# Kernel tuning notes

Hardware: AMD Instinct MI355X
Metric: run time of the kernel (lower is better)

Reference implementation:

```python
import jax, jax.numpy as jnp
import numpy as np

NSTEPS = 8  # scaling-and-squaring steps
SHAPE = (2, 3, 160, 192, 160)  # (batch, ndim, D, H, W)


def _pull3d_wrap(img, coords):
    """Trilinear grid_pull with 'dft' (circular) bound, extrapolate=False.

    img:    (B, D, H, W, C) values
    coords: (B, D, H, W, 3) sampling coordinates in voxels (z, y, x order)
    """
    B, D, H, W, C = img.shape
    c0 = jnp.floor(coords)
    f = coords - c0                       # fractional part, differentiable
    c0 = c0.astype(jnp.int32)
    img_flat = img.reshape(B, D * H * W, C)
    out = jnp.zeros_like(img)
    for dz in (0, 1):
        wz = f[..., 0] if dz else (1.0 - f[..., 0])
        z = jnp.mod(c0[..., 0] + dz, D)
        for dy in (0, 1):
            wy = f[..., 1] if dy else (1.0 - f[..., 1])
            y = jnp.mod(c0[..., 1] + dy, H)
            for dx in (0, 1):
                wx = f[..., 2] if dx else (1.0 - f[..., 2])
                x = jnp.mod(c0[..., 2] + dx, W)
                idx = (z * H + y) * W + x          # (B, D, H, W)
                vals = jnp.take_along_axis(img_flat, idx.reshape(B, -1, 1), axis=1)
                vals = vals.reshape(B, D, H, W, C)
                out = out + vals * (wz * wy * wx)[..., None]
    # extrapolate=False: zero where sample lies outside voxel centers [0, n-1]
    nmax = jnp.asarray([D - 1, H - 1, W - 1], dtype=coords.dtype)
    inb = jnp.all((coords >= 0.0) & (coords <= nmax), axis=-1)
    return jnp.where(inb[..., None], out, 0.0)


def setup_inputs() -> dict:
    key = jax.random.key(0)
    flow = jax.random.normal(key, SHAPE, dtype=jnp.float32)
    return {"flow": flow}


def reference(flow) -> jnp.ndarray:
    """FlowExp forward (interpolation='linear', bound='dft', extrapolate=False,
    coeff=False). Linear spline coefficients == values, so ValueToCoeff /
    CoeffToValue are identities and the loop is pure composition:
        v <- grid_pull(v, identity_grid + v)
    """
    v = jnp.moveaxis(flow, 1, -1) / (2 ** NSTEPS)   # (B, D, H, W, 3)
    B, D, H, W, _ = v.shape
    gz, gy, gx = jnp.meshgrid(
        jnp.arange(D, dtype=v.dtype),
        jnp.arange(H, dtype=v.dtype),
        jnp.arange(W, dtype=v.dtype),
        indexing="ij",
    )
    grid = jnp.stack([gz, gy, gx], axis=-1)          # identity grid (D,H,W,3)
    for _ in range(NSTEPS):
        v = _pull3d_wrap(v, grid[None] + v)
    return jnp.moveaxis(v, -1, 1)                    # (B, 3, D, H, W)
```

## Files before the change

### kernel.cpp

```cpp
#include <hip/hip_runtime.h>


#define BB 2
#define DD 160
#define HH 192
#define WW 160

constexpr int HW    = HH * WW;
constexpr int PLANE = DD * HW;
constexpr int TX = 32, TY = 8, TZ = 8;
constexpr int SX = TX + 2, SY = TY + 2, SZ = TZ + 2;
constexpr int SYX  = SY * SX;
constexpr int SLICE   = 3 * SYX;
constexpr int SLICE_P = 1024;
constexpr int LDSF = SZ * SLICE_P;

constexpr int GX = WW / TX;
constexpr int GY = HH / TY;
constexpr int GZ = (DD / TZ) * BB;
constexpr int NBLK  = GX * GY * GZ;
constexpr int CHUNK = NBLK / 8;

__device__ __forceinline__ void gld_lds4(const float* g, float* l) {
    __builtin_amdgcn_global_load_lds(
        (const __attribute__((address_space(1))) void*)g,
        (__attribute__((address_space(3))) void*)l, 4, 0, 0);
}

__device__ __forceinline__ void tile_coords(int& x0, int& y0, int& z0, int& b) {
    const int lid = blockIdx.x + GX * (blockIdx.y + GY * blockIdx.z);
    const int nl  = (lid & 7) * CHUNK + (lid >> 3);
    const int bx  = nl % GX;
    int r = nl / GX;
    const int by  = r % GY;
    r /= GY;
    b  = r / (DD / TZ);
    x0 = bx * TX;
    y0 = by * TY;
    z0 = (r % (DD / TZ)) * TZ;
}

__device__ __forceinline__ int row_term(int syi, int sxi, int x0, int y0,
                                        bool border) {
    if (!border) return (y0 - 1 + syi) * WW + (x0 - 1 + sxi);
    const int gy = min(max(y0 - 1 + syi, 0), HH - 1);
    const int gx = min(max(x0 - 1 + sxi, 0), WW - 1);
    return gy * WW + gx;
}

__global__ __launch_bounds__(256, 4) void flow_first(const float* __restrict__ vin,
                                                     float* __restrict__ vout,
                                                     float scale) {
    __shared__ float lds[LDSF];
    const int tid = threadIdx.x;
    int x0, y0, z0, b;
    tile_coords(x0, y0, z0, b);
    const bool border = (x0 == 0) | (x0 + TX >= WW) |
                        (y0 == 0) | (y0 + TY >= HH) |
                        (z0 == 0) | (z0 + TZ >= DD);
    const float* vb = vin + b * 3 * PLANE;

    int g0, g1, g2, g3;
    {
        const int l0 = tid;
        int v = l0 / 3, c = l0 - v * 3, a = v / SX;
        g0 = c * PLANE + row_term(a, v - a * SX, x0, y0, border);
        const int l1 = tid + 256;
        v = l1 / 3; c = l1 - v * 3; a = v / SX;
        g1 = c * PLANE + row_term(a, v - a * SX, x0, y0, border);
        const int l2 = tid + 512;
        v = l2 / 3; c = l2 - v * 3; a = v / SX;
        g2 = c * PLANE + row_term(a, v - a * SX, x0, y0, border);
        const int l3 = min(tid + 768, SLICE - 1);
        v = l3 / 3; c = l3 - v * 3; a = v / SX;
        g3 = c * PLANE + row_term(a, v - a * SX, x0, y0, border);
    }

    #pragma unroll
    for (int szi = 0; szi < SZ; ++szi) {
        int zb = z0 - 1 + szi;
        if (border) zb = min(max(zb, 0), DD - 1);
        const float* sp = vb + zb * HW;
        float* lb = lds + szi * SLICE_P;
        gld_lds4(sp + g0, lb + tid);
        gld_lds4(sp + g1, lb + tid + 256);
        gld_lds4(sp + g2, lb + tid + 512);
        gld_lds4(sp + g3, lb + tid + 768);
    }
    __syncthreads();

    const int tx = tid & (TX - 1), ty = tid >> 5;
    const int x = x0 + tx, y = y0 + ty;
    #pragma unroll 2
    for (int zz = 0; zz < TZ; ++zz) {
        const int z = z0 + zz;
        const int so = (zz + 1) * SLICE_P + 3 * ((ty + 1) * SX + (tx + 1));
        const float vz = lds[so] * scale;
        const float vy = lds[so + 1] * scale;
        const float vx = lds[so + 2] * scale;
        const float cz = (float)z + vz, cy = (float)y + vy, cx = (float)x + vx;
        const bool jz = vz < 0.f, jy = vy < 0.f, jx = vx < 0.f;
        const float gzf = jz ? vz + 1.f : vz;
        const float gyf = jy ? vy + 1.f : vy;
        const float gxf = jx ? vx + 1.f : vx;
        const bool inb = (cz >= 0.f) & (cz <= (float)(DD - 1)) &
                         (cy >= 0.f) & (cy <= (float)(HH - 1)) &
                         (cx >= 0.f) & (cx <= (float)(WW - 1));
        const float m = inb ? 1.f : 0.f;
        const float wz1 = gzf * m, wz0 = m - wz1;
        const float wy1 = gyf, wy0 = 1.f - gyf;
        const float wx1 = gxf, wx0 = 1.f - gxf;
        const int sb = ((so - (jx ? 3 : 0)) - (jy ? 3 * SX : 0))
                       - (jz ? SLICE_P : 0);
        float oz = 0.f, oy = 0.f, ox = 0.f;
        #pragma unroll
        for (int dz = 0; dz < 2; ++dz) {
            const float wzv = dz ? wz1 : wz0;
            #pragma unroll
            for (int dy = 0; dy < 2; ++dy) {
                const float wzy = wzv * (dy ? wy1 : wy0);
                const float w0 = wzy * wx0, w1 = wzy * wx1;
                const int o = sb + dz * SLICE_P + dy * (3 * SX);
                oz += lds[o]     * w0; oy += lds[o + 1] * w0; ox += lds[o + 2] * w0;
                oz += lds[o + 3] * w1; oy += lds[o + 4] * w1; ox += lds[o + 5] * w1;
            }
        }
        float t[3] = { oz * scale, oy * scale, ox * scale };
        __builtin_memcpy(vout + (((b * DD + z) * HH + y) * WW + x) * 3, t, 12);
    }
}

template<int OUT_PLANAR>
__global__ __launch_bounds__(256, 4) void flow_mid(const float* __restrict__ vin,
                                                   float* __restrict__ vout) {
    __shared__ float lds[LDSF];
    const int tid = threadIdx.x;
    int x0, y0, z0, b;
    tile_coords(x0, y0, z0, b);
    const bool border = (x0 == 0) | (x0 + TX >= WW) |
                        (y0 == 0) | (y0 + TY >= HH) |
                        (z0 == 0) | (z0 + TZ >= DD);
    const float* vb = vin + b * PLANE * 3;

    int g0, g1, g2, g3;
    {
        const int l0 = tid;
        int v = l0 / 3, c = l0 - v * 3, a = v / SX;
        g0 = row_term(a, v - a * SX, x0, y0, border) * 3 + c;
        const int l1 = tid + 256;
        v = l1 / 3; c = l1 - v * 3; a = v / SX;
        g1 = row_term(a, v - a * SX, x0, y0, border) * 3 + c;
        const int l2 = tid + 512;
        v = l2 / 3; c = l2 - v * 3; a = v / SX;
        g2 = row_term(a, v - a * SX, x0, y0, border) * 3 + c;
        const int l3 = min(tid + 768, SLICE - 1);
        v = l3 / 3; c = l3 - v * 3; a = v / SX;
        g3 = row_term(a, v - a * SX, x0, y0, border) * 3 + c;
    }

    #pragma unroll
    for (int szi = 0; szi < SZ; ++szi) {
        int zb = z0 - 1 + szi;
        if (border) zb = min(max(zb, 0), DD - 1);
        const float* sp = vb + zb * (HW * 3);
        float* lb = lds + szi * SLICE_P;
        gld_lds4(sp + g0, lb + tid);
        gld_lds4(sp + g1, lb + tid + 256);
        gld_lds4(sp + g2, lb + tid + 512);
        gld_lds4(sp + g3, lb + tid + 768);
    }
    __syncthreads();

    const int tx = tid & (TX - 1), ty = tid >> 5;
    const int x = x0 + tx, y = y0 + ty;
    #pragma unroll 2
    for (int zz = 0; zz < TZ; ++zz) {
        const int z = z0 + zz;
        const int so = (zz + 1) * SLICE_P + 3 * ((ty + 1) * SX + (tx + 1));
        const float vz = lds[so], vy = lds[so + 1], vx = lds[so + 2];
        const float cz = (float)z + vz, cy = (float)y + vy, cx = (float)x + vx;
        const bool jz = vz < 0.f, jy = vy < 0.f, jx = vx < 0.f;
        const float gzf = jz ? vz + 1.f : vz;
        const float gyf = jy ? vy + 1.f : vy;
        const float gxf = jx ? vx + 1.f : vx;
        const bool inb = (cz >= 0.f) & (cz <= (float)(DD - 1)) &
                         (cy >= 0.f) & (cy <= (float)(HH - 1)) &
                         (cx >= 0.f) & (cx <= (float)(WW - 1));
        const float m = inb ? 1.f : 0.f;
        const float wz1 = gzf * m, wz0 = m - wz1;
        const float wy1 = gyf, wy0 = 1.f - gyf;
        const float wx1 = gxf, wx0 = 1.f - gxf;
        const int sb = ((so - (jx ? 3 : 0)) - (jy ? 3 * SX : 0))
                       - (jz ? SLICE_P : 0);
        float oz = 0.f, oy = 0.f, ox = 0.f;
        #pragma unroll
        for (int dz = 0; dz < 2; ++dz) {
            const float wzv = dz ? wz1 : wz0;
            #pragma unroll
            for (int dy = 0; dy < 2; ++dy) {
                const float wzy = wzv * (dy ? wy1 : wy0);
                const float w0 = wzy * wx0, w1 = wzy * wx1;
                const int o = sb + dz * SLICE_P + dy * (3 * SX);
                oz += lds[o]     * w0; oy += lds[o + 1] * w0; ox += lds[o + 2] * w0;
                oz += lds[o + 3] * w1; oy += lds[o + 4] * w1; ox += lds[o + 5] * w1;
            }
        }
        if (OUT_PLANAR) {
            float* op = vout + b * 3 * PLANE + (z * HH + y) * WW + x;
            op[0] = oz; op[PLANE] = oy; op[2 * PLANE] = ox;
        } else {
            float t[3] = { oz, oy, ox };
            __builtin_memcpy(vout + (((b * DD + z) * HH + y) * WW + x) * 3, t, 12);
        }
    }
}

extern "C" void kernel_launch(void* const* d_in, const int* in_sizes, int n_in,
                              void* d_out, int out_size, void* d_ws, size_t ws_size,
                              hipStream_t stream) {
    const float* flow = (const float*)d_in[0];
    float* out = (float*)d_out;
    float* wsA = (float*)d_ws;

    dim3 blk(256);
    dim3 grd(GX, GY, GZ);
    const float s = 1.f / 256.f;

    flow_first<<<grd, blk, 0, stream>>>(flow, wsA, s);
    flow_mid<0><<<grd, blk, 0, stream>>>(wsA, out);
    flow_mid<0><<<grd, blk, 0, stream>>>(out, wsA);
    flow_mid<0><<<grd, blk, 0, stream>>>(wsA, out);
    flow_mid<0><<<grd, blk, 0, stream>>>(out, wsA);
    flow_mid<0><<<grd, blk, 0, stream>>>(wsA, out);
    flow_mid<0><<<grd, blk, 0, stream>>>(out, wsA);
    flow_mid<1><<<grd, blk, 0, stream>>>(wsA, out);
}
```

Measured before the change: 397.6 us.

## Pad LDS halo to float4 per voxel and halve z-tile depth

Changes the shared-memory halo layout from 3 floats per voxel to 4, so each corner fetch in the trilinear gather becomes one 16-byte LDS read instead of three scalar reads. To stay within the LDS budget, the z tile depth drops from 8 to 4, which doubles the block count and raises the halo overhead ratio (6 loaded slices per 4 output slices). The gather and store code is factored into a shared template, and the z loop is fully unrolled.

```diff
diff --git a/kernel.cpp b/kernel.cpp
--- a/kernel.cpp
+++ b/kernel.cpp
@@ -8,12 +8,12 @@
 
 constexpr int HW    = HH * WW;
 constexpr int PLANE = DD * HW;
-constexpr int TX = 32, TY = 8, TZ = 8;
+constexpr int TX = 32, TY = 8, TZ = 4;
 constexpr int SX = TX + 2, SY = TY + 2, SZ = TZ + 2;
 constexpr int SYX  = SY * SX;
-constexpr int SLICE   = 3 * SYX;
-constexpr int SLICE_P = 1024;
-constexpr int LDSF = SZ * SLICE_P;
+constexpr int SLICE_P4 = 1536;
+constexpr int LDSF = SZ * SLICE_P4;
+constexpr int KITER = SLICE_P4 / 256;
 
 constexpr int GX = WW / TX;
 constexpr int GY = HH / TY;
@@ -48,56 +48,19 @@
     return gy * WW + gx;
 }
 
-__global__ __launch_bounds__(256, 4) void flow_first(const float* __restrict__ vin,
-                                                     float* __restrict__ vout,
-                                                     float scale) {
-    __shared__ float lds[LDSF];
-    const int tid = threadIdx.x;
-    int x0, y0, z0, b;
-    tile_coords(x0, y0, z0, b);
-    const bool border = (x0 == 0) | (x0 + TX >= WW) |
-                        (y0 == 0) | (y0 + TY >= HH) |
-                        (z0 == 0) | (z0 + TZ >= DD);
-    const float* vb = vin + b * 3 * PLANE;
-
-    int g0, g1, g2, g3;
-    {
-        const int l0 = tid;
-        int v = l0 / 3, c = l0 - v * 3, a = v / SX;
-        g0 = c * PLANE + row_term(a, v - a * SX, x0, y0, border);
-        const int l1 = tid + 256;
-        v = l1 / 3; c = l1 - v * 3; a = v / SX;
-        g1 = c * PLANE + row_term(a, v - a * SX, x0, y0, border);
-        const int l2 = tid + 512;
-        v = l2 / 3; c = l2 - v * 3; a = v / SX;
-        g2 = c * PLANE + row_term(a, v - a * SX, x0, y0, border);
-        const int l3 = min(tid + 768, SLICE - 1);
-        v = l3 / 3; c = l3 - v * 3; a = v / SX;
-        g3 = c * PLANE + row_term(a, v - a * SX, x0, y0, border);
-    }
-
-    #pragma unroll
-    for (int szi = 0; szi < SZ; ++szi) {
-        int zb = z0 - 1 + szi;
-        if (border) zb = min(max(zb, 0), DD - 1);
-        const float* sp = vb + zb * HW;
-        float* lb = lds + szi * SLICE_P;
-        gld_lds4(sp + g0, lb + tid);
-        gld_lds4(sp + g1, lb + tid + 256);
-        gld_lds4(sp + g2, lb + tid + 512);
-        gld_lds4(sp + g3, lb + tid + 768);
-    }
-    __syncthreads();
-
+template<int IN_FIRST, int OUT_PLANAR>
+__device__ __forceinline__ void gather_store(const float* lds, float* vout,
+                                             int x0, int y0, int z0, int b,
+                                             int tid, float scale) {
     const int tx = tid & (TX - 1), ty = tid >> 5;
     const int x = x0 + tx, y = y0 + ty;
-    #pragma unroll 2
+    #pragma unroll
     for (int zz = 0; zz < TZ; ++zz) {
         const int z = z0 + zz;
-        const int so = (zz + 1) * SLICE_P + 3 * ((ty + 1) * SX + (tx + 1));
-        const float vz = lds[so] * scale;
-        const float vy = lds[so + 1] * scale;
-        const float vx = lds[so + 2] * scale;
+        const int so = (zz + 1) * SLICE_P4 + 4 * ((ty + 1) * SX + (tx + 1));
+        const float4 own = *(const float4*)&lds[so];
+        float vz = own.x, vy = own.y, vx = own.z;
+        if (IN_FIRST) { vz *= scale; vy *= scale; vx *= scale; }
         const float cz = (float)z + vz, cy = (float)y + vy, cx = (float)x + vx;
         const bool jz = vz < 0.f, jy = vy < 0.f, jx = vx < 0.f;
         const float gzf = jz ? vz + 1.f : vz;
@@ -110,8 +73,8 @@
         const float wz1 = gzf * m, wz0 = m - wz1;
         const float wy1 = gyf, wy0 = 1.f - gyf;
         const float wx1 = gxf, wx0 = 1.f - gxf;
-        const int sb = ((so - (jx ? 3 : 0)) - (jy ? 3 * SX : 0))
-                       - (jz ? SLICE_P : 0);
+        const int sb = ((so - (jx ? 4 : 0)) - (jy ? 4 * SX : 0))
+                       - (jz ? SLICE_P4 : 0);
         float oz = 0.f, oy = 0.f, ox = 0.f;
         #pragma unroll
         for (int dz = 0; dz < 2; ++dz) {
@@ -120,20 +83,65 @@
             for (int dy = 0; dy < 2; ++dy) {
                 const float wzy = wzv * (dy ? wy1 : wy0);
                 const float w0 = wzy * wx0, w1 = wzy * wx1;
-                const int o = sb + dz * SLICE_P + dy * (3 * SX);
-                oz += lds[o]     * w0; oy += lds[o + 1] * w0; ox += lds[o + 2] * w0;
-                oz += lds[o + 3] * w1; oy += lds[o + 4] * w1; ox += lds[o + 5] * w1;
+                const int o = sb + dz * SLICE_P4 + dy * (4 * SX);
+                const float4 c0 = *(const float4*)&lds[o];
+                const float4 c1 = *(const float4*)&lds[o + 4];
+                oz += c0.x * w0; oy += c0.y * w0; ox += c0.z * w0;
+                oz += c1.x * w1; oy += c1.y * w1; ox += c1.z * w1;
             }
         }
-        float t[3] = { oz * scale, oy * scale, ox * scale };
-        __builtin_memcpy(vout + (((b * DD + z) * HH + y) * WW + x) * 3, t, 12);
+        if (IN_FIRST) { oz *= scale; oy *= scale; ox *= scale; }
+        if (OUT_PLANAR) {
+            float* op = vout + b * 3 * PLANE + (z * HH + y) * WW + x;
+            op[0] = oz; op[PLANE] = oy; op[2 * PLANE] = ox;
+        } else {
+            float t[3] = { oz, oy, ox };
+            __builtin_memcpy(vout + (((b * DD + z) * HH + y) * WW + x) * 3,
+                             t, 12);
+        }
     }
+}
+
+__global__ __launch_bounds__(256, 4) void flow_first(const float* __restrict__ vin,
+                                                     float* __restrict__ vout,
+                                                     float scale) {
+    __shared__ __align__(16) float lds[LDSF];
+    const int tid = threadIdx.x;
+    int x0, y0, z0, b;
+    tile_coords(x0, y0, z0, b);
+    const bool border = (x0 == 0) | (x0 + TX >= WW) |
+                        (y0 == 0) | (y0 + TY >= HH) |
+                        (z0 == 0) | (z0 + TZ >= DD);
+    const float* vb = vin + b * 3 * PLANE;
+
+    int g[KITER];
+    #pragma unroll
+    for (int k = 0; k < KITER; ++k) {
+        const int L = tid + k * 256;
+        const int vox = min(L >> 2, SYX - 1);
+        const int ch  = min(L & 3, 2);
+        const int a = vox / SX;
+        g[k] = ch * PLANE + row_term(a, vox - a * SX, x0, y0, border);
+    }
+
+    #pragma unroll
+    for (int szi = 0; szi < SZ; ++szi) {
+        int zb = z0 - 1 + szi;
+        if (border) zb = min(max(zb, 0), DD - 1);
+        const float* sp = vb + zb * HW;
+        float* lb = lds + szi * SLICE_P4;
+        #pragma unroll
+        for (int k = 0; k < KITER; ++k)
+            gld_lds4(sp + g[k], lb + tid + k * 256);
+    }
+    __syncthreads();
+    gather_store<1, 0>(lds, vout, x0, y0, z0, b, tid, scale);
 }
 
 template<int OUT_PLANAR>
 __global__ __launch_bounds__(256, 4) void flow_mid(const float* __restrict__ vin,
                                                    float* __restrict__ vout) {
-    __shared__ float lds[LDSF];
+    __shared__ __align__(16) float lds[LDSF];
     const int tid = threadIdx.x;
     int x0, y0, z0, b;
     tile_coords(x0, y0, z0, b);
@@ -142,20 +150,14 @@
                         (z0 == 0) | (z0 + TZ >= DD);
     const float* vb = vin + b * PLANE * 3;
 
-    int g0, g1, g2, g3;
-    {
-        const int l0 = tid;
-        int v = l0 / 3, c = l0 - v * 3, a = v / SX;
-        g0 = row_term(a, v - a * SX, x0, y0, border) * 3 + c;
-        const int l1 = tid + 256;
-        v = l1 / 3; c = l1 - v * 3; a = v / SX;
-        g1 = row_term(a, v - a * SX, x0, y0, border) * 3 + c;
-        const int l2 = tid + 512;
-        v = l2 / 3; c = l2 - v * 3; a = v / SX;
-        g2 = row_term(a, v - a * SX, x0, y0, border) * 3 + c;
-        const int l3 = min(tid + 768, SLICE - 1);
-        v = l3 / 3; c = l3 - v * 3; a = v / SX;
-        g3 = row_term(a, v - a * SX, x0, y0, border) * 3 + c;
+    int g[KITER];
+    #pragma unroll
+    for (int k = 0; k < KITER; ++k) {
+        const int L = tid + k * 256;
+        const int vox = min(L >> 2, SYX - 1);
+        const int ch  = min(L & 3, 2);
+        const int a = vox / SX;
+        g[k] = row_term(a, vox - a * SX, x0, y0, border) * 3 + ch;
     }
 
     #pragma unroll
@@ -163,56 +165,13 @@
         int zb = z0 - 1 + szi;
         if (border) zb = min(max(zb, 0), DD - 1);
         const float* sp = vb + zb * (HW * 3);
-        float* lb = lds + szi * SLICE_P;
-        gld_lds4(sp + g0, lb + tid);
-        gld_lds4(sp + g1, lb + tid + 256);
-        gld_lds4(sp + g2, lb + tid + 512);
-        gld_lds4(sp + g3, lb + tid + 768);
+        float* lb = lds + szi * SLICE_P4;
+        #pragma unroll
+        for (int k = 0; k < KITER; ++k)
+            gld_lds4(sp + g[k], lb + tid + k * 256);
     }
     __syncthreads();
-
-    const int tx = tid & (TX - 1), ty = tid >> 5;
-    const int x = x0 + tx, y = y0 + ty;
-    #pragma unroll 2
-    for (int zz = 0; zz < TZ; ++zz) {
-        const int z = z0 + zz;
-        const int so = (zz + 1) * SLICE_P + 3 * ((ty + 1) * SX + (tx + 1));
-        const float vz = lds[so], vy = lds[so + 1], vx = lds[so + 2];
-        const float cz = (float)z + vz, cy = (float)y + vy, cx = (float)x + vx;
-        const bool jz = vz < 0.f, jy = vy < 0.f, jx = vx < 0.f;
-        const float gzf = jz ? vz + 1.f : vz;
-        const float gyf = jy ? vy + 1.f : vy;
-        const float gxf = jx ? vx + 1.f : vx;
-        const bool inb = (cz >= 0.f) & (cz <= (float)(DD - 1)) &
-                         (cy >= 0.f) & (cy <= (float)(HH - 1)) &
-                         (cx >= 0.f) & (cx <= (float)(WW - 1));
-        const float m = inb ? 1.f : 0.f;
-        const float wz1 = gzf * m, wz0 = m - wz1;
-        const float wy1 = gyf, wy0 = 1.f - gyf;
-        const float wx1 = gxf, wx0 = 1.f - gxf;
-        const int sb = ((so - (jx ? 3 : 0)) - (jy ? 3 * SX : 0))
-                       - (jz ? SLICE_P : 0);
-        float oz = 0.f, oy = 0.f, ox = 0.f;
-        #pragma unroll
-        for (int dz = 0; dz < 2; ++dz) {
-            const float wzv = dz ? wz1 : wz0;
-            #pragma unroll
-            for (int dy = 0; dy < 2; ++dy) {
-                const float wzy = wzv * (dy ? wy1 : wy0);
-                const float w0 = wzy * wx0, w1 = wzy * wx1;
-                const int o = sb + dz * SLICE_P + dy * (3 * SX);
-                oz += lds[o]     * w0; oy += lds[o + 1] * w0; ox += lds[o + 2] * w0;
-                oz += lds[o + 3] * w1; oy += lds[o + 4] * w1; ox += lds[o + 5] * w1;
-            }
-        }
-        if (OUT_PLANAR) {
-            float* op = vout + b * 3 * PLANE + (z * HH + y) * WW + x;
-            op[0] = oz; op[PLANE] = oy; op[2 * PLANE] = ox;
-        } else {
-            float t[3] = { oz, oy, ox };
-            __builtin_memcpy(vout + (((b * DD + z) * HH + y) * WW + x) * 3, t, 12);
-        }
-    }
+    gather_store<0, OUT_PLANAR>(lds, vout, x0, y0, z0, b, tid, 1.f);
 }
 
 extern "C" void kernel_launch(void* const* d_in, const int* in_sizes, int n_in,
```

Result: slower. 424.4 us (+6.7%).
